# Optimization experiments

Hardware: AMD Instinct MI355X
Metric: run time of the kernel (lower is better)

## Reference

```python
import jax, jax.numpy as jnp
import numpy as np

K = 20
EPS = 1e-5  # BatchNorm eps
SLOPE = 0.2  # LeakyReLU negative slope


def _lrelu(y):
    return jnp.where(y > 0, y, SLOPE * y)


def _knn_idx(x):
    # x: [B, C, N] -> idx [B, N, K] of nearest neighbors (largest of negative sq dist)
    inner = -2.0 * jnp.einsum('bcn,bcm->bnm', x, x)
    xx = jnp.sum(x * x, axis=1)  # [B, N]
    pd = -xx[:, :, None] - inner - xx[:, None, :]  # [B, N, N]
    return jax.lax.top_k(pd, K)[1]


def _graph_feature(x):
    # x: [B, C, N] -> [B, 2C, N, K] = cat(neighbor - center, center)
    idx = _knn_idx(x)
    xt = jnp.transpose(x, (0, 2, 1))  # [B, N, C]
    nb = jax.vmap(lambda f, i: f[i])(xt, idx)  # [B, N, K, C]
    ctr = xt[:, :, None, :]
    feat = jnp.concatenate([nb - ctr, jnp.broadcast_to(ctr, nb.shape)], axis=-1)
    return jnp.transpose(feat, (0, 3, 1, 2))


def _bn(y, p, ch_axis):
    g, b, m, v = p[0], p[1], p[2], p[3]
    shape = [1] * y.ndim
    shape[ch_axis] = -1
    scale = (g / jnp.sqrt(v + EPS)).reshape(shape)
    return (y - m.reshape(shape)) * scale + b.reshape(shape)


def _conv_block(x, w, bn):
    f = _graph_feature(x)  # [B, 2C_in, N, K]
    y = jnp.einsum('bcnk,oc->bonk', f, w)  # 1x1 conv, no bias
    y = _lrelu(_bn(y, bn, 1))
    return jnp.max(y, axis=-1)  # max over K neighbors -> [B, C_out, N]


def setup_inputs() -> dict:
    key = jax.random.key(0)
    ks = jax.random.split(key, 20)
    B, N = 8, 1024
    inp = {
        'x': jax.random.normal(ks[0], (B, 3, N), jnp.float32),
        'w0': jax.random.normal(ks[1], (64, 6), jnp.float32) * 0.1,
        'w1': jax.random.normal(ks[2], (64, 128), jnp.float32) * 0.1,
        'w2': jax.random.normal(ks[3], (128, 128), jnp.float32) * 0.1,
        'w3': jax.random.normal(ks[4], (256, 256), jnp.float32) * 0.1,
        'bn0': jax.random.uniform(ks[5], (4, 64), jnp.float32) + 0.1,
        'bn1': jax.random.uniform(ks[6], (4, 64), jnp.float32) + 0.1,
        'bn2': jax.random.uniform(ks[7], (4, 128), jnp.float32) + 0.1,
        'bn3': jax.random.uniform(ks[8], (4, 256), jnp.float32) + 0.1,
        'we': jax.random.normal(ks[9], (1024, 512), jnp.float32) * 0.05,
        'bne': jax.random.uniform(ks[10], (4, 1024), jnp.float32) + 0.1,
        'wf0': jax.random.normal(ks[11], (512, 2048), jnp.float32) * 0.02,
        'bnf0': jax.random.uniform(ks[12], (4, 512), jnp.float32) + 0.1,
        'wf1': jax.random.normal(ks[13], (256, 512), jnp.float32) * 0.05,
        'bnf1': jax.random.uniform(ks[14], (4, 256), jnp.float32) + 0.1,
        'wfin': jax.random.normal(ks[15], (64, 256), jnp.float32) * 0.05,
        'bfin': jax.random.normal(ks[16], (64,), jnp.float32) * 0.05,
    }
    return inp


def reference(x, w0, w1, w2, w3, bn0, bn1, bn2, bn3, we, bne, wf0, bnf0, wf1, bnf1, wfin, bfin):
    B = x.shape[0]
    x1 = _conv_block(x, w0, bn0)   # [B, 64, N]
    x2 = _conv_block(x1, w1, bn1)  # [B, 64, N]
    x3 = _conv_block(x2, w2, bn2)  # [B, 128, N]
    x4 = _conv_block(x3, w3, bn3)  # [B, 256, N]
    cat = jnp.concatenate([x1, x2, x3, x4], axis=1)  # [B, 512, N]
    e = _lrelu(_bn(jnp.einsum('bcn,oc->bon', cat, we), bne, 1))  # [B, 1024, N]
    p1 = jnp.max(e, axis=-1)
    p2 = jnp.mean(e, axis=-1)
    h = jnp.concatenate([p1, p2], axis=1)  # [B, 2048]
    h = _lrelu(_bn(h @ wf0.T, bnf0, 1))  # [B, 512]; dropout is eval-mode identity
    h = _lrelu(_bn(h @ wf1.T, bnf1, 1))  # [B, 256]
    return h @ wfin.T + bfin  # [B, 64]
```

## Files before the change

### kernel.cpp

```cpp
#include <hip/hip_runtime.h>
#include <math.h>

#define N_PTS 1024
#define BATCH 8
#define KNN 20
#define EPSB 1e-5f
#define SLOPE 0.2f

typedef __attribute__((ext_vector_type(8))) short short8;
typedef __attribute__((ext_vector_type(4))) float f32x4;
typedef unsigned short ushort_t;
typedef unsigned long long u64;

__device__ __forceinline__ float lrelu(float y) { return y > 0.f ? y : SLOPE * y; }

__device__ __forceinline__ ushort_t f2bf(float f) {
    union { float f; unsigned u; } v; v.f = f;
    unsigned r = v.u + 0x7FFF + ((v.u >> 16) & 1);
    return (ushort_t)(r >> 16);
}

__device__ __forceinline__ void wprep_one(const float* __restrict__ w, float* __restrict__ wpt,
                                          int C, int Cout, int g) {
    int M2 = 2 * Cout;
    if (g >= C * M2) return;
    int c = g / M2, m = g - c * M2;
    float v;
    if (m < Cout) v = w[(size_t)m * 2 * C + c];
    else { int o = m - Cout; v = w[(size_t)o * 2 * C + C + c] - w[(size_t)o * 2 * C + c]; }
    wpt[(size_t)c * M2 + m] = v;
}

__global__ void prep_kernel(const float* __restrict__ we, ushort_t* __restrict__ weh,
                            const float* __restrict__ w0, float* __restrict__ wpt0,
                            const float* __restrict__ w1, float* __restrict__ wpt1,
                            const float* __restrict__ w2, float* __restrict__ wpt2,
                            const float* __restrict__ w3, float* __restrict__ wpt3) {
    int bx = blockIdx.x, tid = threadIdx.x;
    if (bx < 512) {
        int g = bx * 256 + tid;
        float4 v = ((const float4*)we)[g];
        ushort4 o;
        o.x = f2bf(v.x); o.y = f2bf(v.y); o.z = f2bf(v.z); o.w = f2bf(v.w);
        ((ushort4*)weh)[g] = o;
    } else if (bx < 514) {
        wprep_one(w0, wpt0, 3, 64, (bx - 512) * 256 + tid);
    } else if (bx < 546) {
        wprep_one(w1, wpt1, 64, 64, (bx - 514) * 256 + tid);
    } else if (bx < 610) {
        wprep_one(w2, wpt2, 64, 128, (bx - 546) * 256 + tid);
    } else {
        wprep_one(w3, wpt3, 128, 256, (bx - 610) * 256 + tid);
    }
}

__global__ void __launch_bounds__(256)
pdabv_kernel(const float* __restrict__ x, const float* __restrict__ wpt,
             float* __restrict__ pd, float* __restrict__ A, float* __restrict__ Bv,
             int C, int Cout, int bstride) {
    int b = blockIdx.z;
    int nt = blockIdx.y;
    int bx = blockIdx.x;
    int tid = threadIdx.x;
    int tx = tid & 15, ty = tid >> 4;
    int n0 = nt * 128;
    __shared__ float sU0[16][128];
    __shared__ float sU1[16][128];
    __shared__ float sXX[256];
    const float* xb = x + (size_t)b * bstride;
    float acc[8][8] = {};
    if (bx < 8) {
        int m0 = bx * 128;
        float xxa = 0.f;
        for (int c0 = 0; c0 < C; c0 += 16) {
            for (int q = 0; q < 2; q++) {
                int f = q * 256 + tid;
                int r = f >> 5, col = (f & 31) * 4;
                int c = c0 + r;
                float4 vn = {0.f, 0.f, 0.f, 0.f}, vm = {0.f, 0.f, 0.f, 0.f};
                if (c < C) {
                    vn = *(const float4*)&xb[(size_t)c * N_PTS + n0 + col];
                    vm = *(const float4*)&xb[(size_t)c * N_PTS + m0 + col];
                }
                *(float4*)&sU0[r][col] = vn;
                *(float4*)&sU1[r][col] = vm;
            }
            __syncthreads();
            if (tid < 128) {
                for (int k = 0; k < 16; k++) { float v = sU0[k][tid]; xxa += v * v; }
            } else {
                int u = tid - 128;
                for (int k = 0; k < 16; k++) { float v = sU1[k][u]; xxa += v * v; }
            }
            for (int k = 0; k < 16; k++) {
                float4 a0 = *(const float4*)&sU0[k][ty * 4];
                float4 a1 = *(const float4*)&sU0[k][64 + ty * 4];
                float4 b0 = *(const float4*)&sU1[k][tx * 4];
                float4 b1 = *(const float4*)&sU1[k][64 + tx * 4];
                float av[8] = {a0.x, a0.y, a0.z, a0.w, a1.x, a1.y, a1.z, a1.w};
                float bw[8] = {b0.x, b0.y, b0.z, b0.w, b1.x, b1.y, b1.z, b1.w};
                for (int i = 0; i < 8; i++)
                    for (int j = 0; j < 8; j++) acc[i][j] += av[i] * bw[j];
            }
            __syncthreads();
        }
        sXX[tid] = xxa;
        __syncthreads();
        float xnv[8], xmv[8];
        for (int i = 0; i < 8; i++) xnv[i] = sXX[(i >> 2) * 64 + ty * 4 + (i & 3)];
        for (int j = 0; j < 8; j++) xmv[j] = sXX[128 + (j >> 2) * 64 + tx * 4 + (j & 3)];
        for (int i = 0; i < 8; i++) {
            int n = n0 + (i >> 2) * 64 + ty * 4 + (i & 3);
            float* prow = pd + ((size_t)(b * N_PTS + n)) * N_PTS;
            for (int jh = 0; jh < 2; jh++) {
                float4 o;
                o.x = 2.f * acc[i][jh * 4 + 0] - xnv[i] - xmv[jh * 4 + 0];
                o.y = 2.f * acc[i][jh * 4 + 1] - xnv[i] - xmv[jh * 4 + 1];
                o.z = 2.f * acc[i][jh * 4 + 2] - xnv[i] - xmv[jh * 4 + 2];
                o.w = 2.f * acc[i][jh * 4 + 3] - xnv[i] - xmv[jh * 4 + 3];
                *(float4*)&prow[m0 + jh * 64 + tx * 4] = o;
            }
        }
    } else {
        int m0 = (bx - 8) * 128;
        int M2 = 2 * Cout;
        for (int c0 = 0; c0 < C; c0 += 16) {
            for (int q = 0; q < 2; q++) {
                int f = q * 256 + tid;
                int r = f >> 5, col = (f & 31) * 4;
                int c = c0 + r;
                float4 vw = {0.f, 0.f, 0.f, 0.f}, vx = {0.f, 0.f, 0.f, 0.f};
                if (c < C) {
                    vw = *(const float4*)&wpt[(size_t)c * M2 + m0 + col];
                    vx = *(const float4*)&xb[(size_t)c * N_PTS + n0 + col];
                }
                *(float4*)&sU0[r][col] = vw;
                *(float4*)&sU1[r][col] = vx;
            }
            __syncthreads();
            for (int k = 0; k < 16; k++) {
                float4 a0 = *(const float4*)&sU0[k][ty * 4];
                float4 a1 = *(const float4*)&sU0[k][64 + ty * 4];
                float4 b0 = *(const float4*)&sU1[k][tx * 4];
                float4 b1 = *(const float4*)&sU1[k][64 + tx * 4];
                float av[8] = {a0.x, a0.y, a0.z, a0.w, a1.x, a1.y, a1.z, a1.w};
                float bw[8] = {b0.x, b0.y, b0.z, b0.w, b1.x, b1.y, b1.z, b1.w};
                for (int i = 0; i < 8; i++)
                    for (int j = 0; j < 8; j++) acc[i][j] += av[i] * bw[j];
            }
            __syncthreads();
        }
        for (int i = 0; i < 8; i++) {
            int rowm = m0 + (i >> 2) * 64 + ty * 4 + (i & 3);
            float* dst = (rowm < Cout) ? (A + ((size_t)b * Cout + rowm) * N_PTS)
                                       : (Bv + ((size_t)b * Cout + rowm - Cout) * N_PTS);
            for (int jh = 0; jh < 2; jh++) {
                float4 o;
                o.x = acc[i][jh * 4 + 0];
                o.y = acc[i][jh * 4 + 1];
                o.z = acc[i][jh * 4 + 2];
                o.w = acc[i][jh * 4 + 3];
                *(float4*)&dst[n0 + jh * 64 + tx * 4] = o;
            }
        }
    }
}

__global__ void __launch_bounds__(256)
topk_kernel(const float* __restrict__ pd, int* __restrict__ idx) {
    int wid = threadIdx.x >> 6;
    int row = blockIdx.x * 4 + wid;
    int lane = threadIdx.x & 63;
    __shared__ u64 Sk[4][64];
    const float* p = pd + (size_t)row * N_PTS;
    float v[16];
    for (int q = 0; q < 4; q++) {
        float4 t = *(const float4*)&p[lane * 16 + q * 4];
        v[q * 4 + 0] = t.x; v[q * 4 + 1] = t.y; v[q * 4 + 2] = t.z; v[q * 4 + 3] = t.w;
    }
    float lmax = v[0];
    #pragma unroll
    for (int j = 1; j < 16; j++) lmax = fmaxf(lmax, v[j]);
    float s = lmax;
    #pragma unroll
    for (int k = 2; k <= 64; k <<= 1) {
        #pragma unroll
        for (int j = k >> 1; j > 0; j >>= 1) {
            float o = __shfl_xor(s, j, 64);
            bool takeMin = (((lane & k) == 0) == ((lane & j) == 0));
            float mn = fminf(s, o), mx = fmaxf(s, o);
            s = takeMin ? mn : mx;
        }
    }
    float tp = __shfl(s, 44, 64);
    unsigned hm = 0;
    #pragma unroll
    for (int j = 0; j < 16; j++) hm |= (v[j] >= tp ? 1u : 0u) << j;
    int cnt = __popc(hm);
    int incl = cnt;
    #pragma unroll
    for (int d = 1; d < 64; d <<= 1) {
        int o = __shfl_up(incl, d, 64);
        if (lane >= d) incl += o;
    }
    int total = __shfl(incl, 63, 64);
    int pos = incl - cnt;
    if (total <= 64) {
        #pragma unroll
        for (int j = 0; j < 16; j++) {
            if (hm & (1u << j)) {
                unsigned u = __float_as_uint(v[j]);
                unsigned msk = ((unsigned)((int)u >> 31)) | 0x80000000u;
                Sk[wid][pos] = ((u64)(u ^ msk) << 32) | (unsigned)(1023 - (lane * 16 + j));
                pos++;
            }
        }
        u64 key = (lane < total) ? Sk[wid][lane] : 0ull;
        #pragma unroll
        for (int k = 2; k <= 64; k <<= 1) {
            #pragma unroll
            for (int j = k >> 1; j > 0; j >>= 1) {
                u64 o = __shfl_xor(key, j, 64);
                bool takeMin = (((lane & k) == 0) == ((lane & j) == 0));
                bool sgt = key > o;
                key = (sgt != takeMin) ? key : o;
            }
        }
        if (lane >= 44) {
            int m = 1023 - (int)(unsigned)(key & 0xFFFFFFFFu);
            idx[row * KNN + (63 - lane)] = m;
        }
    } else {
        for (int kk = 0; kk < KNN; kk++) {
            float bv = v[0]; int bj = 0;
            #pragma unroll
            for (int j = 1; j < 16; j++) if (v[j] > bv) { bv = v[j]; bj = j; }
            int bi = lane * 16 + bj;
            for (int d = 32; d > 0; d >>= 1) {
                float ov = __shfl_down(bv, d, 64);
                int oi = __shfl_down(bi, d, 64);
                if (ov > bv || (ov == bv && oi < bi)) { bv = ov; bi = oi; }
            }
            bi = __shfl(bi, 0, 64);
            if ((bi >> 4) == lane) {
                #pragma unroll
                for (int j = 0; j < 16; j++) if (j == (bi & 15)) v[j] = -INFINITY;
            }
            if (lane == 0) idx[row * KNN + kk] = bi;
        }
    }
}

__global__ void __launch_bounds__(256)
gmax_kernel(const float* __restrict__ A, const float* __restrict__ Bv,
            const int* __restrict__ idx, const float* __restrict__ bnp,
            float* __restrict__ out, int Cout, int outStrideB) {
    int b = blockIdx.z;
    int n0 = blockIdx.x * 64;
    int o0 = blockIdx.y * 4;
    int tid = threadIdx.x;
    __shared__ int sidx[64 * 21];
    __shared__ float sA[4][N_PTS];
    for (int t = tid; t < 64 * KNN; t += 256) {
        int nl = t / KNN, k = t - nl * KNN;
        sidx[nl * 21 + k] = idx[(b * N_PTS + n0) * KNN + t];
    }
    const float* Abase = A + ((size_t)b * Cout + o0) * N_PTS;
    for (int q = 0; q < 4; q++) {
        int f = q * 256 + tid;
        int r = f >> 8, c4 = (f & 255) * 4;
        *(float4*)&sA[r][c4] = *(const float4*)&Abase[(size_t)r * N_PTS + c4];
    }
    __syncthreads();
    int nl = tid & 63, ol = tid >> 6;
    float best = -INFINITY;
    #pragma unroll
    for (int k = 0; k < KNN; k++) {
        int j = sidx[nl * 21 + k];
        best = fmaxf(best, sA[ol][j]);
    }
    int o = o0 + ol;
    int n = n0 + nl;
    float pre = best + Bv[((size_t)b * Cout + o) * N_PTS + n];
    float g = bnp[o], bb = bnp[Cout + o], m = bnp[2 * Cout + o], vv = bnp[3 * Cout + o];
    float scale = g / sqrtf(vv + EPSB);
    out[(size_t)b * outStrideB + (size_t)o * N_PTS + n] = lrelu((pre - m) * scale + bb);
}

__global__ void catT_kernel(const float* __restrict__ cat, ushort_t* __restrict__ catT) {
    int b = blockIdx.z, ct = blockIdx.y, nt = blockIdx.x;
    int tid = threadIdx.x;
    __shared__ float tile[64][65];
    const float* cb = cat + (size_t)b * 512 * N_PTS;
    for (int q = 0; q < 16; q++) {
        int e = q * 256 + tid;
        int c = e >> 6, n = e & 63;
        tile[c][n] = cb[(size_t)(ct * 64 + c) * N_PTS + nt * 64 + n];
    }
    __syncthreads();
    for (int q = 0; q < 16; q++) {
        int e = q * 256 + tid;
        int n = e >> 6, c = e & 63;
        catT[((size_t)b * N_PTS + nt * 64 + n) * 512 + ct * 64 + c] = f2bf(tile[c][n]);
    }
}

__global__ void __launch_bounds__(256)
gemm6_mfma(const ushort_t* __restrict__ weh, const ushort_t* __restrict__ catT,
           const float* __restrict__ bne,
           float* __restrict__ pmax, float* __restrict__ psum) {
    int b = blockIdx.z, ot = blockIdx.y, nt = blockIdx.x;
    int tid = threadIdx.x;
    int w = tid >> 6, lane = tid & 63, q = lane >> 4, lr = lane & 15;
    int mblk = w >> 1, nblk = w & 1;
    __shared__ __align__(16) ushort_t sA[128 * 40];
    __shared__ __align__(16) ushort_t sB[128 * 40];
    __shared__ float sa[128], sc[128];
    __shared__ float redmax[128][2], redsum[128][2];
    int o0 = ot * 128, n0 = nt * 128;
    if (tid < 128) {
        int o = o0 + tid;
        float g = bne[o], bb = bne[1024 + o], m = bne[2048 + o], vv = bne[3072 + o];
        float scale = g / sqrtf(vv + EPSB);
        sa[tid] = scale; sc[tid] = bb - m * scale;
    }
    f32x4 acc[4][4] = {};
    const ushort_t* cT = catT + (size_t)b * N_PTS * 512;
    int r0 = tid >> 2, s = tid & 3;
    for (int k0 = 0; k0 < 512; k0 += 32) {
        __syncthreads();
        for (int h = 0; h < 2; h++) {
            int r = r0 + h * 64;
            *(short8*)&sA[r * 40 + s * 8] = *(const short8*)(weh + (size_t)(o0 + r) * 512 + k0 + s * 8);
            *(short8*)&sB[r * 40 + s * 8] = *(const short8*)(cT  + (size_t)(n0 + r) * 512 + k0 + s * 8);
        }
        __syncthreads();
        short8 af[4], bfr[4];
        for (int mi = 0; mi < 4; mi++)
            af[mi] = *(const short8*)&sA[(mblk * 64 + mi * 16 + lr) * 40 + q * 8];
        for (int ni = 0; ni < 4; ni++)
            bfr[ni] = *(const short8*)&sB[(nblk * 64 + ni * 16 + lr) * 40 + q * 8];
        for (int mi = 0; mi < 4; mi++)
            for (int ni = 0; ni < 4; ni++)
                acc[mi][ni] = __builtin_amdgcn_mfma_f32_16x16x32_bf16(af[mi], bfr[ni], acc[mi][ni], 0, 0, 0);
    }
    for (int mi = 0; mi < 4; mi++) {
        for (int r = 0; r < 4; r++) {
            int row = mblk * 64 + mi * 16 + q * 4 + r;
            float a = sa[row], c = sc[row];
            float mx = -INFINITY, sm = 0.f;
            for (int ni = 0; ni < 4; ni++) {
                float y = lrelu(acc[mi][ni][r] * a + c);
                mx = fmaxf(mx, y); sm += y;
            }
            for (int msk = 1; msk < 16; msk <<= 1) {
                mx = fmaxf(mx, __shfl_xor(mx, msk, 16));
                sm += __shfl_xor(sm, msk, 16);
            }
            if (lr == 0) { redmax[row][nblk] = mx; redsum[row][nblk] = sm; }
        }
    }
    __syncthreads();
    if (tid < 128) {
        float mx = fmaxf(redmax[tid][0], redmax[tid][1]);
        float sm = redsum[tid][0] + redsum[tid][1];
        int o = o0 + tid;
        pmax[((size_t)(b * 1024 + o)) * 8 + nt] = mx;
        psum[((size_t)(b * 1024 + o)) * 8 + nt] = sm;
    }
}

__global__ void pool_reduce_kernel(const float* __restrict__ pmax, const float* __restrict__ psum,
                                   float* __restrict__ h0) {
    int g = blockIdx.x * 256 + threadIdx.x;
    int b = g >> 10, o = g & 1023;
    float mx = -INFINITY, sm = 0.f;
    for (int t = 0; t < 8; t++) { mx = fmaxf(mx, pmax[g * 8 + t]); sm += psum[g * 8 + t]; }
    h0[(size_t)b * 2048 + o] = mx;
    h0[(size_t)b * 2048 + 1024 + o] = sm * (1.0f / 1024.0f);
}

__global__ void fc_kernel(const float* __restrict__ in, const float* __restrict__ w,
                          const float* __restrict__ bnp, const float* __restrict__ bias,
                          float* __restrict__ out, int Cin, int Cout, int mode) {
    int blk = blockIdx.x;
    int b = blk / Cout, o = blk % Cout;
    int lane = threadIdx.x;
    const float* inb = in + (size_t)b * Cin;
    const float* wo = w + (size_t)o * Cin;
    float acc = 0.f;
    for (int c = lane; c < Cin; c += 64) acc += inb[c] * wo[c];
    for (int s = 32; s > 0; s >>= 1) acc += __shfl_down(acc, s, 64);
    if (lane == 0) {
        float y = acc;
        if (mode == 0) {
            float g = bnp[o], bb = bnp[Cout + o], m = bnp[2 * Cout + o], vv = bnp[3 * Cout + o];
            y = lrelu((y - m) * (g / sqrtf(vv + EPSB)) + bb);
        } else {
            y += bias[o];
        }
        out[(size_t)b * Cout + o] = y;
    }
}

extern "C" void kernel_launch(void* const* d_in, const int* in_sizes, int n_in,
                              void* d_out, int out_size, void* d_ws, size_t ws_size,
                              hipStream_t stream) {
    const float* x    = (const float*)d_in[0];
    const float* w0   = (const float*)d_in[1];
    const float* w1   = (const float*)d_in[2];
    const float* w2   = (const float*)d_in[3];
    const float* w3   = (const float*)d_in[4];
    const float* bn0  = (const float*)d_in[5];
    const float* bn1  = (const float*)d_in[6];
    const float* bn2  = (const float*)d_in[7];
    const float* bn3  = (const float*)d_in[8];
    const float* we   = (const float*)d_in[9];
    const float* bne  = (const float*)d_in[10];
    const float* wf0  = (const float*)d_in[11];
    const float* bnf0 = (const float*)d_in[12];
    const float* wf1  = (const float*)d_in[13];
    const float* bnf1 = (const float*)d_in[14];
    const float* wfin = (const float*)d_in[15];
    const float* bfin = (const float*)d_in[16];

    float* ws = (float*)d_ws;
    size_t off = 0;
    float* cat  = ws + off; off += (size_t)BATCH * 512 * N_PTS;
    float* pd   = ws + off; off += (size_t)BATCH * N_PTS * N_PTS;
    float* A    = ws + off; off += (size_t)BATCH * 256 * N_PTS;
    float* Bv   = ws + off; off += (size_t)BATCH * 256 * N_PTS;
    float* pmax = ws + off; off += (size_t)BATCH * N_PTS * 8;
    float* psum = ws + off; off += (size_t)BATCH * N_PTS * 8;
    float* h0   = ws + off; off += (size_t)BATCH * 2048;
    float* h1   = ws + off; off += (size_t)BATCH * 512;
    float* h2   = ws + off; off += (size_t)BATCH * 256;
    int*   idx  = (int*)(ws + off); off += (size_t)BATCH * N_PTS * KNN;
    ushort_t* weh  = (ushort_t*)(ws + off); off += (size_t)(1024 * 512) / 2;
    ushort_t* catT = (ushort_t*)(ws + off); off += (size_t)BATCH * N_PTS * 512 / 2;
    float* wpt0 = ws + off; off += 3 * 128;
    float* wpt1 = ws + off; off += 64 * 128;
    float* wpt2 = ws + off; off += 64 * 256;
    float* wpt3 = ws + off; off += 128 * 512;

    const int CSTR = 512 * N_PTS;
    const int topkBlocks = BATCH * N_PTS / 4;

    prep_kernel<<<866, 256, 0, stream>>>(we, weh, w0, wpt0, w1, wpt1, w2, wpt2, w3, wpt3);

    pdabv_kernel<<<dim3(9, 8, BATCH), 256, 0, stream>>>(x, wpt0, pd, A, Bv, 3, 64, 3 * N_PTS);
    topk_kernel<<<topkBlocks, 256, 0, stream>>>(pd, idx);
    gmax_kernel<<<dim3(16, 16, BATCH), 256, 0, stream>>>(A, Bv, idx, bn0, cat, 64, CSTR);

    pdabv_kernel<<<dim3(9, 8, BATCH), 256, 0, stream>>>(cat, wpt1, pd, A, Bv, 64, 64, CSTR);
    topk_kernel<<<topkBlocks, 256, 0, stream>>>(pd, idx);
    gmax_kernel<<<dim3(16, 16, BATCH), 256, 0, stream>>>(A, Bv, idx, bn1, cat + 64 * N_PTS, 64, CSTR);

    pdabv_kernel<<<dim3(10, 8, BATCH), 256, 0, stream>>>(cat + 64 * N_PTS, wpt2, pd, A, Bv, 64, 128, CSTR);
    topk_kernel<<<topkBlocks, 256, 0, stream>>>(pd, idx);
    gmax_kernel<<<dim3(16, 32, BATCH), 256, 0, stream>>>(A, Bv, idx, bn2, cat + 128 * N_PTS, 128, CSTR);

    pdabv_kernel<<<dim3(12, 8, BATCH), 256, 0, stream>>>(cat + 128 * N_PTS, wpt3, pd, A, Bv, 128, 256, CSTR);
    topk_kernel<<<topkBlocks, 256, 0, stream>>>(pd, idx);
    gmax_kernel<<<dim3(16, 64, BATCH), 256, 0, stream>>>(A, Bv, idx, bn3, cat + 256 * N_PTS, 256, CSTR);

    catT_kernel<<<dim3(16, 8, BATCH), 256, 0, stream>>>(cat, catT);
    gemm6_mfma<<<dim3(8, 8, BATCH), 256, 0, stream>>>(weh, catT, bne, pmax, psum);
    pool_reduce_kernel<<<32, 256, 0, stream>>>(pmax, psum, h0);

    fc_kernel<<<BATCH * 512, 64, 0, stream>>>(h0, wf0, bnf0, nullptr, h1, 2048, 512, 0);
    fc_kernel<<<BATCH * 256, 64, 0, stream>>>(h1, wf1, bnf1, nullptr, h2, 512, 256, 0);
    fc_kernel<<<BATCH * 64, 64, 0, stream>>>(h2, wfin, nullptr, bfin, (float*)d_out, 256, 64, 1);
}
```

Before: 331.6 us.

## Fuse first-layer kNN distances into top-k and drop row-constant norm term

For the first layer (C=3), a new top-k kernel computes the distance scores directly from the input points, so the full pairwise-distance matrix is no longer written and re-read. The pd kernel now launches only the A/B tiles for that layer. In the later layers, the per-row norm term is dropped because it is constant along a row and cannot change top-k order. The column norms now come from a small separate xx kernel instead of being accumulated inside the GEMM tile. This adds three small launches and changes pd values, but only by a per-row offset.

```diff
diff --git a/kernel.cpp b/kernel.cpp
--- a/kernel.cpp
+++ b/kernel.cpp
@@ -54,10 +54,22 @@
     }
 }
 
+__global__ void __launch_bounds__(64)
+xx_kernel(const float* __restrict__ x, float* __restrict__ xx, int C, int bstride) {
+    int b = blockIdx.y;
+    int n = blockIdx.x * 64 + threadIdx.x;
+    const float* xb = x + (size_t)b * bstride + n;
+    float s = 0.f;
+    #pragma unroll 4
+    for (int c = 0; c < C; c++) { float v = xb[(size_t)c * N_PTS]; s += v * v; }
+    xx[b * N_PTS + n] = s;
+}
+
 __global__ void __launch_bounds__(256)
 pdabv_kernel(const float* __restrict__ x, const float* __restrict__ wpt,
+             const float* __restrict__ xx,
              float* __restrict__ pd, float* __restrict__ A, float* __restrict__ Bv,
-             int C, int Cout, int bstride) {
+             int C, int Cout, int bstride, int pdTiles) {
     int b = blockIdx.z;
     int nt = blockIdx.y;
     int bx = blockIdx.x;
@@ -66,12 +78,10 @@
     int n0 = nt * 128;
     __shared__ float sU0[16][128];
     __shared__ float sU1[16][128];
-    __shared__ float sXX[256];
     const float* xb = x + (size_t)b * bstride;
     float acc[8][8] = {};
-    if (bx < 8) {
+    if (bx < pdTiles) {
         int m0 = bx * 128;
-        float xxa = 0.f;
         for (int c0 = 0; c0 < C; c0 += 16) {
             for (int q = 0; q < 2; q++) {
                 int f = q * 256 + tid;
@@ -86,12 +96,6 @@
                 *(float4*)&sU1[r][col] = vm;
             }
             __syncthreads();
-            if (tid < 128) {
-                for (int k = 0; k < 16; k++) { float v = sU0[k][tid]; xxa += v * v; }
-            } else {
-                int u = tid - 128;
-                for (int k = 0; k < 16; k++) { float v = sU1[k][u]; xxa += v * v; }
-            }
             for (int k = 0; k < 16; k++) {
                 float4 a0 = *(const float4*)&sU0[k][ty * 4];
                 float4 a1 = *(const float4*)&sU0[k][64 + ty * 4];
@@ -104,25 +108,24 @@
             }
             __syncthreads();
         }
-        sXX[tid] = xxa;
-        __syncthreads();
-        float xnv[8], xmv[8];
-        for (int i = 0; i < 8; i++) xnv[i] = sXX[(i >> 2) * 64 + ty * 4 + (i & 3)];
-        for (int j = 0; j < 8; j++) xmv[j] = sXX[128 + (j >> 2) * 64 + tx * 4 + (j & 3)];
+        float xm[8];
+        const float* xxb = xx + b * N_PTS + m0;
+        *(float4*)&xm[0] = *(const float4*)&xxb[tx * 4];
+        *(float4*)&xm[4] = *(const float4*)&xxb[64 + tx * 4];
         for (int i = 0; i < 8; i++) {
             int n = n0 + (i >> 2) * 64 + ty * 4 + (i & 3);
             float* prow = pd + ((size_t)(b * N_PTS + n)) * N_PTS;
             for (int jh = 0; jh < 2; jh++) {
                 float4 o;
-                o.x = 2.f * acc[i][jh * 4 + 0] - xnv[i] - xmv[jh * 4 + 0];
-                o.y = 2.f * acc[i][jh * 4 + 1] - xnv[i] - xmv[jh * 4 + 1];
-                o.z = 2.f * acc[i][jh * 4 + 2] - xnv[i] - xmv[jh * 4 + 2];
-                o.w = 2.f * acc[i][jh * 4 + 3] - xnv[i] - xmv[jh * 4 + 3];
+                o.x = 2.f * acc[i][jh * 4 + 0] - xm[jh * 4 + 0];
+                o.y = 2.f * acc[i][jh * 4 + 1] - xm[jh * 4 + 1];
+                o.z = 2.f * acc[i][jh * 4 + 2] - xm[jh * 4 + 2];
+                o.w = 2.f * acc[i][jh * 4 + 3] - xm[jh * 4 + 3];
                 *(float4*)&prow[m0 + jh * 64 + tx * 4] = o;
             }
         }
     } else {
-        int m0 = (bx - 8) * 128;
+        int m0 = (bx - pdTiles) * 128;
         int M2 = 2 * Cout;
         for (int c0 = 0; c0 < C; c0 += 16) {
             for (int q = 0; q < 2; q++) {
@@ -177,6 +180,106 @@
     for (int q = 0; q < 4; q++) {
         float4 t = *(const float4*)&p[lane * 16 + q * 4];
         v[q * 4 + 0] = t.x; v[q * 4 + 1] = t.y; v[q * 4 + 2] = t.z; v[q * 4 + 3] = t.w;
+    }
+    float lmax = v[0];
+    #pragma unroll
+    for (int j = 1; j < 16; j++) lmax = fmaxf(lmax, v[j]);
+    float s = lmax;
+    #pragma unroll
+    for (int k = 2; k <= 64; k <<= 1) {
+        #pragma unroll
+        for (int j = k >> 1; j > 0; j >>= 1) {
+            float o = __shfl_xor(s, j, 64);
+            bool takeMin = (((lane & k) == 0) == ((lane & j) == 0));
+            float mn = fminf(s, o), mx = fmaxf(s, o);
+            s = takeMin ? mn : mx;
+        }
+    }
+    float tp = __shfl(s, 44, 64);
+    unsigned hm = 0;
+    #pragma unroll
+    for (int j = 0; j < 16; j++) hm |= (v[j] >= tp ? 1u : 0u) << j;
+    int cnt = __popc(hm);
+    int incl = cnt;
+    #pragma unroll
+    for (int d = 1; d < 64; d <<= 1) {
+        int o = __shfl_up(incl, d, 64);
+        if (lane >= d) incl += o;
+    }
+    int total = __shfl(incl, 63, 64);
+    int pos = incl - cnt;
+    if (total <= 64) {
+        #pragma unroll
+        for (int j = 0; j < 16; j++) {
+            if (hm & (1u << j)) {
+                unsigned u = __float_as_uint(v[j]);
+                unsigned msk = ((unsigned)((int)u >> 31)) | 0x80000000u;
+                Sk[wid][pos] = ((u64)(u ^ msk) << 32) | (unsigned)(1023 - (lane * 16 + j));
+                pos++;
+            }
+        }
+        u64 key = (lane < total) ? Sk[wid][lane] : 0ull;
+        #pragma unroll
+        for (int k = 2; k <= 64; k <<= 1) {
+            #pragma unroll
+            for (int j = k >> 1; j > 0; j >>= 1) {
+                u64 o = __shfl_xor(key, j, 64);
+                bool takeMin = (((lane & k) == 0) == ((lane & j) == 0));
+                bool sgt = key > o;
+                key = (sgt != takeMin) ? key : o;
+            }
+        }
+        if (lane >= 44) {
+            int m = 1023 - (int)(unsigned)(key & 0xFFFFFFFFu);
+            idx[row * KNN + (63 - lane)] = m;
+        }
+    } else {
+        for (int kk = 0; kk < KNN; kk++) {
+            float bv = v[0]; int bj = 0;
+            #pragma unroll
+            for (int j = 1; j < 16; j++) if (v[j] > bv) { bv = v[j]; bj = j; }
+            int bi = lane * 16 + bj;
+            for (int d = 32; d > 0; d >>= 1) {
+                float ov = __shfl_down(bv, d, 64);
+                int oi = __shfl_down(bi, d, 64);
+                if (ov > bv || (ov == bv && oi < bi)) { bv = ov; bi = oi; }
+            }
+            bi = __shfl(bi, 0, 64);
+            if ((bi >> 4) == lane) {
+                #pragma unroll
+                for (int j = 0; j < 16; j++) if (j == (bi & 15)) v[j] = -INFINITY;
+            }
+            if (lane == 0) idx[row * KNN + kk] = bi;
+        }
+    }
+}
+
+__global__ void __launch_bounds__(256)
+topk0_kernel(const float* __restrict__ x, int* __restrict__ idx) {
+    int wid = threadIdx.x >> 6;
+    int row = blockIdx.x * 4 + wid;
+    int lane = threadIdx.x & 63;
+    __shared__ u64 Sk[4][64];
+    int b = row >> 10, n = row & 1023;
+    const float* xb = x + (size_t)b * 3 * N_PTS;
+    float xr0 = xb[n], xr1 = xb[N_PTS + n], xr2 = xb[2 * N_PTS + n];
+    float v[16];
+    for (int q = 0; q < 4; q++) {
+        int base = lane * 16 + q * 4;
+        float4 c0 = *(const float4*)&xb[base];
+        float4 c1 = *(const float4*)&xb[N_PTS + base];
+        float4 c2 = *(const float4*)&xb[2 * N_PTS + base];
+        float a0[4] = {c0.x, c0.y, c0.z, c0.w};
+        float a1[4] = {c1.x, c1.y, c1.z, c1.w};
+        float a2[4] = {c2.x, c2.y, c2.z, c2.w};
+        #pragma unroll
+        for (int j = 0; j < 4; j++) {
+            float d = 0.f;
+            d += xr0 * a0[j]; d += xr1 * a1[j]; d += xr2 * a2[j];
+            float sq = 0.f;
+            sq += a0[j] * a0[j]; sq += a1[j] * a1[j]; sq += a2[j] * a2[j];
+            v[q * 4 + j] = 2.f * d - sq;
+        }
     }
     float lmax = v[0];
     #pragma unroll
@@ -430,6 +533,7 @@
     float* pd   = ws + off; off += (size_t)BATCH * N_PTS * N_PTS;
     float* A    = ws + off; off += (size_t)BATCH * 256 * N_PTS;
     float* Bv   = ws + off; off += (size_t)BATCH * 256 * N_PTS;
+    float* xxv  = ws + off; off += (size_t)BATCH * N_PTS;
     float* pmax = ws + off; off += (size_t)BATCH * N_PTS * 8;
     float* psum = ws + off; off += (size_t)BATCH * N_PTS * 8;
     float* h0   = ws + off; off += (size_t)BATCH * 2048;
@@ -448,19 +552,22 @@
 
     prep_kernel<<<866, 256, 0, stream>>>(we, weh, w0, wpt0, w1, wpt1, w2, wpt2, w3, wpt3);
 
-    pdabv_kernel<<<dim3(9, 8, BATCH), 256, 0, stream>>>(x, wpt0, pd, A, Bv, 3, 64, 3 * N_PTS);
-    topk_kernel<<<topkBlocks, 256, 0, stream>>>(pd, idx);
+    pdabv_kernel<<<dim3(1, 8, BATCH), 256, 0, stream>>>(x, wpt0, xxv, pd, A, Bv, 3, 64, 3 * N_PTS, 0);
+    topk0_kernel<<<topkBlocks, 256, 0, stream>>>(x, idx);
     gmax_kernel<<<dim3(16, 16, BATCH), 256, 0, stream>>>(A, Bv, idx, bn0, cat, 64, CSTR);
 
-    pdabv_kernel<<<dim3(9, 8, BATCH), 256, 0, stream>>>(cat, wpt1, pd, A, Bv, 64, 64, CSTR);
+    xx_kernel<<<dim3(16, BATCH), 64, 0, stream>>>(cat, xxv, 64, CSTR);
+    pdabv_kernel<<<dim3(9, 8, BATCH), 256, 0, stream>>>(cat, wpt1, xxv, pd, A, Bv, 64, 64, CSTR, 8);
     topk_kernel<<<topkBlocks, 256, 0, stream>>>(pd, idx);
     gmax_kernel<<<dim3(16, 16, BATCH), 256, 0, stream>>>(A, Bv, idx, bn1, cat + 64 * N_PTS, 64, CSTR);
 
-    pdabv_kernel<<<dim3(10, 8, BATCH), 256, 0, stream>>>(cat + 64 * N_PTS, wpt2, pd, A, Bv, 64, 128, CSTR);
+    xx_kernel<<<dim3(16, BATCH), 64, 0, stream>>>(cat + 64 * N_PTS, xxv, 64, CSTR);
+    pdabv_kernel<<<dim3(10, 8, BATCH), 256, 0, stream>>>(cat + 64 * N_PTS, wpt2, xxv, pd, A, Bv, 64, 128, CSTR, 8);
     topk_kernel<<<topkBlocks, 256, 0, stream>>>(pd, idx);
     gmax_kernel<<<dim3(16, 32, BATCH), 256, 0, stream>>>(A, Bv, idx, bn2, cat + 128 * N_PTS, 128, CSTR);
 
-    pdabv_kernel<<<dim3(12, 8, BATCH), 256, 0, stream>>>(cat + 128 * N_PTS, wpt3, pd, A, Bv, 128, 256, CSTR);
+    xx_kernel<<<dim3(16, BATCH), 64, 0, stream>>>(cat + 128 * N_PTS, xxv, 128, CSTR);
+    pdabv_kernel<<<dim3(12, 8, BATCH), 256, 0, stream>>>(cat + 128 * N_PTS, wpt3, xxv, pd, A, Bv, 128, 256, CSTR, 8);
     topk_kernel<<<topkBlocks, 256, 0, stream>>>(pd, idx);
     gmax_kernel<<<dim3(16, 64, BATCH), 256, 0, stream>>>(A, Bv, idx, bn3, cat + 256 * N_PTS, 256, CSTR);
 
```

After: 351.0 us. 5.9% more time.
